# Kernel optimization log

Hardware: AMD Instinct MI355X
Metric: run time of the kernel (lower is better)

The kernel has to match this reference:

```python
import jax, jax.numpy as jnp
import numpy as np

NOISE_RATIO = 25
NORM_TERM = 9.0

def setup_inputs() -> dict:
    key = jax.random.key(0)
    k1, k2, k3, k4, k5 = jax.random.split(key, 5)
    N, E, V, K = 4096, 1024, 50257, NOISE_RATIO
    x = jax.random.normal(k1, (N, E), dtype=jnp.float32)
    target = jax.random.randint(k2, (N,), 0, V)
    noise_idx = jax.random.randint(k3, (N, K), 0, V)
    # decoder params per IndexLinear.reset_parameters: weight ~ U(-0.1, 0.1), bias = 0
    weight = jax.random.uniform(k4, (V, E), dtype=jnp.float32, minval=-0.1, maxval=0.1)
    bias = jnp.zeros((V,), dtype=jnp.float32)
    # noise distribution over the vocab (positive, normalized)
    noise = jax.random.uniform(k5, (V,), dtype=jnp.float32, minval=0.1, maxval=1.0)
    noise = noise / jnp.sum(noise)
    return {"x": x, "target": target, "noise_idx": noise_idx,
            "weight": weight, "bias": bias, "noise": noise}

def reference(x, target, noise_idx, weight, bias, noise):
    """NCE loss (training branch), size_average=True.
    x: (N, E), target: (N,), noise_idx: (N, K), weight: (V, E), bias: (V,), noise: (V,)
    """
    N = x.shape[0]
    k = jnp.float32(NOISE_RATIO)
    # IndexLinear: gather rows for [target | noise] then per-sample (1,E)@(E,1+K)
    idx = jnp.concatenate([target[:, None], noise_idx], axis=1)   # (N, 1+K)
    w_rows = weight[idx]                                          # (N, 1+K, E)
    b_rows = bias[idx]                                            # (N, 1+K)
    logits = b_rows + jnp.einsum('ne,nke->nk', x, w_rows)         # (N, 1+K)
    probs = jnp.exp(logits - NORM_TERM)
    data_prob = probs[:, 0]                                       # (N,)
    noise_in_data = probs[:, 1:]                                  # (N, K)
    pn_target = noise[target]                                     # (N,)
    pn_noise = noise[noise_idx]                                   # (N, K)
    rnn_loss = jnp.log(data_prob / (data_prob + k * pn_target))
    noise_loss = jnp.sum(jnp.log(k * pn_noise / (noise_in_data + k * pn_noise)), axis=1)
    loss = -jnp.sum(rnn_loss + noise_loss)
    return loss / N
```

## Files before the change

kernel.cpp:

```cpp
#include <hip/hip_runtime.h>
#include <hip/hip_bf16.h>


#define NN 4096
#define EE 1024
#define KK 25

__device__ __forceinline__ void fma4(float4& a, const float4& p, const float4& q) {
    a.x += p.x * q.x; a.y += p.y * q.y; a.z += p.z * q.z; a.w += p.w * q.w;
}

__global__ __launch_bounds__(256) void nce_main_kernel(
    const float* __restrict__ x,
    const int* __restrict__ target,
    const int* __restrict__ noise_idx,
    const float* __restrict__ weight,
    const float* __restrict__ bias,
    const float* __restrict__ noise,
    float* __restrict__ block_loss)
{
    const int n = blockIdx.x;
    const int wave = threadIdx.x >> 6;
    const int lane = threadIdx.x & 63;

    const float4* x4 = (const float4*)(x + (size_t)n * EE);
    const float4 xr0 = x4[lane];
    const float4 xr1 = x4[64 + lane];
    const float4 xr2 = x4[128 + lane];
    const float4 xr3 = x4[192 + lane];

    const int nj = (wave < 2) ? 7 : 6;

    float sacc[7];
    int rows[7];

#pragma unroll
    for (int jj = 0; jj < 7; ++jj) {
        const int j = wave + (jj << 2);
        const bool valid = (jj < nj);
        int row = 0;
        float4 a = make_float4(0.f, 0.f, 0.f, 0.f);
        if (valid) {
            row = (j == 0) ? target[n] : noise_idx[n * KK + (j - 1)];
            const float4* w4 = (const float4*)(weight + (size_t)row * EE);
            const float4 w0 = w4[lane];
            const float4 w1 = w4[64 + lane];
            const float4 w2 = w4[128 + lane];
            const float4 w3 = w4[192 + lane];
            fma4(a, xr0, w0);
            fma4(a, xr1, w1);
            fma4(a, xr2, w2);
            fma4(a, xr3, w3);
        }
        rows[jj] = row;
        sacc[jj] = (a.x + a.y) + (a.z + a.w);
    }

#pragma unroll
    for (int jj = 0; jj < 7; ++jj) {
#pragma unroll
        for (int off = 32; off > 0; off >>= 1)
            sacc[jj] += __shfl_xor(sacc[jj], off);
    }

    __shared__ float swave[4];
    if (lane == 0) {
        float part = 0.0f;
#pragma unroll
        for (int jj = 0; jj < 7; ++jj) {
            if (jj < nj) {
                const int j = wave + (jj << 2);
                const int row = rows[jj];
                const float logit = sacc[jj] + bias[row];
                const float p = expf(logit - 9.0f);
                const float pn25 = 25.0f * noise[row];
                part += (j == 0) ? logf(p / (p + pn25))
                                 : logf(pn25 / (p + pn25));
            }
        }
        swave[wave] = part;
    }
    __syncthreads();
    if (threadIdx.x == 0)
        block_loss[n] = -((swave[0] + swave[1]) + (swave[2] + swave[3]));
}

__global__ __launch_bounds__(256) void nce_reduce_kernel(
    const float* __restrict__ block_loss, float* __restrict__ out)
{
    float acc = 0.0f;
    for (int i = threadIdx.x; i < NN; i += 256)
        acc += block_loss[i];
#pragma unroll
    for (int off = 32; off > 0; off >>= 1)
        acc += __shfl_down(acc, off);
    __shared__ float s[4];
    const int wave = threadIdx.x >> 6;
    const int lane = threadIdx.x & 63;
    if (lane == 0) s[wave] = acc;
    __syncthreads();
    if (threadIdx.x == 0)
        out[0] = ((s[0] + s[1]) + (s[2] + s[3])) / (float)NN;
}

extern "C" void kernel_launch(void* const* d_in, const int* in_sizes, int n_in,
                              void* d_out, int out_size, void* d_ws, size_t ws_size,
                              hipStream_t stream) {
    const float* x        = (const float*)d_in[0];
    const int*   target   = (const int*)d_in[1];
    const int*   noiseIdx = (const int*)d_in[2];
    const float* weight   = (const float*)d_in[3];
    const float* bias     = (const float*)d_in[4];
    const float* noise    = (const float*)d_in[5];
    float* out = (float*)d_out;
    float* block_loss = (float*)d_ws;

    nce_main_kernel<<<NN, 256, 0, stream>>>(x, target, noiseIdx, weight, bias, noise, block_loss);
    nce_reduce_kernel<<<1, 256, 0, stream>>>(block_loss, out);
}
```

Measured before the change: 315.4 us.

## Prefetch all gathered weight rows into registers and reduce via bucketed atomics

The main kernel now reads all row indices first, then issues every weight-row load (7 rows x 4 float4 per lane) before any FMA, so many gathers are in flight together instead of one row at a time. The per-block shared-memory reduction and barrier are replaced by per-wave atomicAdd into 256 buckets, which are zeroed by a memset and summed by a small 64-thread finalize kernel. The prefetch raises register use (112 floats of weights per lane) and may lower occupancy. The atomics make the summation order non-deterministic, and the extra memset adds a launch.

```diff
diff --git a/kernel.cpp b/kernel.cpp
--- a/kernel.cpp
+++ b/kernel.cpp
@@ -5,6 +5,7 @@
 #define NN 4096
 #define EE 1024
 #define KK 25
+#define NBUCKET 256
 
 __device__ __forceinline__ void fma4(float4& a, const float4& p, const float4& q) {
     a.x += p.x * q.x; a.y += p.y * q.y; a.z += p.z * q.z; a.w += p.w * q.w;
@@ -17,42 +18,41 @@
     const float* __restrict__ weight,
     const float* __restrict__ bias,
     const float* __restrict__ noise,
-    float* __restrict__ block_loss)
+    float* __restrict__ buckets)
 {
     const int n = blockIdx.x;
     const int wave = threadIdx.x >> 6;
     const int lane = threadIdx.x & 63;
 
-    const float4* x4 = (const float4*)(x + (size_t)n * EE);
-    const float4 xr0 = x4[lane];
-    const float4 xr1 = x4[64 + lane];
-    const float4 xr2 = x4[128 + lane];
-    const float4 xr3 = x4[192 + lane];
-
     const int nj = (wave < 2) ? 7 : 6;
 
-    float sacc[7];
     int rows[7];
-
 #pragma unroll
     for (int jj = 0; jj < 7; ++jj) {
         const int j = wave + (jj << 2);
-        const bool valid = (jj < nj);
-        int row = 0;
+        rows[jj] = (jj < nj) ? ((j == 0) ? target[n] : noise_idx[n * KK + (j - 1)])
+                             : 0;
+    }
+
+    const float4* x4 = (const float4*)(x + (size_t)n * EE);
+    float4 xr[4];
+#pragma unroll
+    for (int p = 0; p < 4; ++p) xr[p] = x4[p * 64 + lane];
+
+    float4 wr[7][4];
+#pragma unroll
+    for (int jj = 0; jj < 7; ++jj) {
+        const float4* w4 = (const float4*)(weight + (size_t)rows[jj] * EE);
+#pragma unroll
+        for (int p = 0; p < 4; ++p) wr[jj][p] = w4[p * 64 + lane];
+    }
+
+    float sacc[7];
+#pragma unroll
+    for (int jj = 0; jj < 7; ++jj) {
         float4 a = make_float4(0.f, 0.f, 0.f, 0.f);
-        if (valid) {
-            row = (j == 0) ? target[n] : noise_idx[n * KK + (j - 1)];
-            const float4* w4 = (const float4*)(weight + (size_t)row * EE);
-            const float4 w0 = w4[lane];
-            const float4 w1 = w4[64 + lane];
-            const float4 w2 = w4[128 + lane];
-            const float4 w3 = w4[192 + lane];
-            fma4(a, xr0, w0);
-            fma4(a, xr1, w1);
-            fma4(a, xr2, w2);
-            fma4(a, xr3, w3);
-        }
-        rows[jj] = row;
+#pragma unroll
+        for (int p = 0; p < 4; ++p) fma4(a, xr[p], wr[jj][p]);
         sacc[jj] = (a.x + a.y) + (a.z + a.w);
     }
 
@@ -63,7 +63,6 @@
             sacc[jj] += __shfl_xor(sacc[jj], off);
     }
 
-    __shared__ float swave[4];
     if (lane == 0) {
         float part = 0.0f;
 #pragma unroll
@@ -78,29 +77,20 @@
                                  : logf(pn25 / (p + pn25));
             }
         }
-        swave[wave] = part;
+        atomicAdd(&buckets[(n + wave * 64) & (NBUCKET - 1)], -part);
     }
-    __syncthreads();
-    if (threadIdx.x == 0)
-        block_loss[n] = -((swave[0] + swave[1]) + (swave[2] + swave[3]));
 }
 
-__global__ __launch_bounds__(256) void nce_reduce_kernel(
-    const float* __restrict__ block_loss, float* __restrict__ out)
+__global__ __launch_bounds__(64) void nce_finalize_kernel(
+    const float* __restrict__ buckets, float* __restrict__ out)
 {
-    float acc = 0.0f;
-    for (int i = threadIdx.x; i < NN; i += 256)
-        acc += block_loss[i];
+    float acc = buckets[threadIdx.x] + buckets[threadIdx.x + 64]
+              + buckets[threadIdx.x + 128] + buckets[threadIdx.x + 192];
 #pragma unroll
     for (int off = 32; off > 0; off >>= 1)
-        acc += __shfl_down(acc, off);
-    __shared__ float s[4];
-    const int wave = threadIdx.x >> 6;
-    const int lane = threadIdx.x & 63;
-    if (lane == 0) s[wave] = acc;
-    __syncthreads();
+        acc += __shfl_xor(acc, off);
     if (threadIdx.x == 0)
-        out[0] = ((s[0] + s[1]) + (s[2] + s[3])) / (float)NN;
+        out[0] = acc / (float)NN;
 }
 
 extern "C" void kernel_launch(void* const* d_in, const int* in_sizes, int n_in,
@@ -113,8 +103,9 @@
     const float* bias     = (const float*)d_in[4];
     const float* noise    = (const float*)d_in[5];
     float* out = (float*)d_out;
-    float* block_loss = (float*)d_ws;
+    float* buckets = (float*)d_ws;
 
-    nce_main_kernel<<<NN, 256, 0, stream>>>(x, target, noiseIdx, weight, bias, noise, block_loss);
-    nce_reduce_kernel<<<1, 256, 0, stream>>>(block_loss, out);
+    hipMemsetAsync(buckets, 0, NBUCKET * sizeof(float), stream);
+    nce_main_kernel<<<NN, 256, 0, stream>>>(x, target, noiseIdx, weight, bias, noise, buckets);
+    nce_finalize_kernel<<<1, 64, 0, stream>>>(buckets, out);
 }
```

Measured after the change: 315.4 us. Within noise of the previous version (-0.0%).
